# Kernel tuning notes

Measured on AMD Instinct MI355X. Metric: run time of the kernel, lower is better.

## Reference

```python
import jax, jax.numpy as jnp
import numpy as np

B, N, M, K = 8, 8192, 512, 32
C_IN, EMB = 3, 256
RADIUS2 = 0.1 * 0.1
EPS = 1e-5


def setup_inputs() -> dict:
    key = jax.random.key(0)
    ks = jax.random.split(key, 8)
    p = jax.random.uniform(ks[0], (B, N, 3), dtype=jnp.float32)           # coords in [0,1]^3
    x = jax.random.normal(ks[1], (B, C_IN, N), dtype=jnp.float32)          # features [B,C,N]
    def w(k, co, ci):
        return jax.random.normal(k, (co, ci), dtype=jnp.float32) / np.float32(np.sqrt(ci))
    return {
        "p": p, "x": x,
        # conv1: (6->256, BN+ReLU), (256->256, plain+bias)
        "W0": w(ks[2], EMB, 6), "g0": jnp.ones((EMB,), jnp.float32), "be0": jnp.zeros((EMB,), jnp.float32),
        "W1": w(ks[3], EMB, EMB), "b1": jnp.zeros((EMB,), jnp.float32),
        # conv2 (input doubled to 512): (512->512, BN+ReLU), (512->256, plain+bias)
        "W2": w(ks[4], 2 * EMB, 2 * EMB), "g2": jnp.ones((2 * EMB,), jnp.float32), "be2": jnp.zeros((2 * EMB,), jnp.float32),
        "W3": w(ks[5], EMB, 2 * EMB), "b3": jnp.zeros((EMB,), jnp.float32),
    }


def furthest_point_sample(p, m):
    # p: [B,N,3] -> idx [B,m] int32; starts at index 0 (matches CUDA FPS)
    b, n, _ = p.shape
    def step(carry, _):
        min_d, last = carry
        last_pt = jnp.take_along_axis(p, last[:, None, None], axis=1)     # [B,1,3]
        d = jnp.sum((p - last_pt) ** 2, axis=-1)                           # [B,N]
        min_d = jnp.minimum(min_d, d)
        nxt = jnp.argmax(min_d, axis=-1).astype(jnp.int32)
        return (min_d, nxt), last
    init = (jnp.full((b, n), 1e10, p.dtype), jnp.zeros((b,), jnp.int32))
    _, idx = jax.lax.scan(step, init, None, length=m)
    return idx.T                                                           # [B,m]


def ball_query(center_p, p, k, r2):
    # first-k-in-order points within radius; pad with first valid (center is always valid)
    d2 = jnp.sum((center_p[:, :, None, :] - p[:, None, :, :]) ** 2, axis=-1)  # [B,M,N]
    n = p.shape[1]
    keyv = jnp.where(d2 < r2, jnp.arange(n, dtype=jnp.int32), jnp.int32(n))   # [B,M,N]
    keys = jnp.sort(keyv, axis=-1)[..., :k]                                    # [B,M,K]
    valid = keys < n
    idx = jnp.where(valid, keys, keys[..., 0:1])
    return idx.astype(jnp.int32)


def bn_relu(f, g, b):
    # training-mode BatchNorm2d over (B, M, K) per channel, then ReLU
    mu = jnp.mean(f, axis=(0, 2, 3), keepdims=True)
    var = jnp.var(f, axis=(0, 2, 3), keepdims=True)
    fh = (f - mu) * jax.lax.rsqrt(var + EPS)
    return jax.nn.relu(fh * g[None, :, None, None] + b[None, :, None, None])


def reference(p, x, W0, g0, be0, W1, b1, W2, g2, be2, W3, b3):
    idx = furthest_point_sample(p, M)                                       # [B,M]
    center_p = jnp.take_along_axis(p, idx[:, :, None], axis=1)              # [B,M,3]
    gidx = ball_query(center_p, p, K, RADIUS2)                              # [B,M,K]
    grouped_xyz = jax.vmap(lambda pts, ix: pts[ix])(p, gidx)                # [B,M,K,3]
    dp = jnp.transpose(grouped_xyz - center_p[:, :, None, :], (0, 3, 1, 2))  # [B,3,M,K]
    fj = jax.vmap(lambda ft, ix: ft[:, ix])(x, gidx)                        # [B,C,M,K]
    center_x = jnp.take_along_axis(x, idx[:, None, :], axis=2)              # [B,C,M]
    f = jnp.concatenate([dp, fj - center_x[..., None]], axis=1)             # [B,6,M,K]  (dp_df)
    # conv1
    f = bn_relu(jnp.einsum('oc,bcmk->bomk', W0, f), g0, be0)
    f = jnp.einsum('oc,bcmk->bomk', W1, f) + b1[None, :, None, None]
    # mid max-pool concat
    fmax = jnp.max(f, axis=-1, keepdims=True)
    f = jnp.concatenate([jnp.broadcast_to(fmax, f.shape), f], axis=1)       # [B,512,M,K]
    # conv2
    f = bn_relu(jnp.einsum('oc,bcmk->bomk', W2, f), g2, be2)
    f = jnp.einsum('oc,bcmk->bomk', W3, f) + b3[None, :, None, None]
    out_f = jnp.max(f, axis=-1)                                             # [B,256,M]
    return (p, center_p, x, out_f)
```

## Files before the change

### kernel.cpp

```cpp
#include <hip/hip_runtime.h>

typedef unsigned short u16;
typedef unsigned int u32;
typedef unsigned long long u64;
typedef __bf16 bf16x8 __attribute__((ext_vector_type(8)));
typedef float v4f32 __attribute__((ext_vector_type(4)));

#define NP 8192
#define NM 512
#define LTOT 131072
#define NBM 4096
#define R2F 0.009999999776482582f

__device__ __forceinline__ float bf2f(u16 u) { return __uint_as_float(((u32)u) << 16); }
__device__ __forceinline__ u16 f2bf(float f) {
  u32 u = __float_as_uint(f);
  return (u16)((u + 0x7fffu + ((u >> 16) & 1u)) >> 16);
}
__device__ __forceinline__ void gl16(const void* g, void* l) {
  __builtin_amdgcn_global_load_lds((const __attribute__((address_space(1))) u32*)g,
                                   (__attribute__((address_space(3))) u32*)l, 16, 0, 0);
}

__device__ __forceinline__ u64 wave_max64_dpp(u64 k) {
#define DPP_STEP(CTRL) { \
    u32 lo_ = (u32)__builtin_amdgcn_update_dpp(0, (int)(u32)k, CTRL, 0xF, 0xF, true); \
    u32 hi_ = (u32)__builtin_amdgcn_update_dpp(0, (int)(u32)(k >> 32), CTRL, 0xF, 0xF, true); \
    u64 o_ = ((u64)hi_ << 32) | lo_; \
    if (o_ > k) k = o_; }
  DPP_STEP(0x111)
  DPP_STEP(0x112)
  DPP_STEP(0x114)
  DPP_STEP(0x118)
  DPP_STEP(0x142)
  DPP_STEP(0x143)
#undef DPP_STEP
  return k;
}

#define MFMA_COMPUTE_P(ASP, BSP) do { \
  bf16x8 a_[4], b_[4]; \
  _Pragma("unroll") \
  for (int mi_ = 0; mi_ < 4; ++mi_) a_[mi_] = *(const bf16x8*)&(ASP)[(wrow + mi_*16 + l15)*32 + l4*8]; \
  _Pragma("unroll") \
  for (int ni_ = 0; ni_ < 4; ++ni_) b_[ni_] = *(const bf16x8*)&(BSP)[(wcol + ni_*16 + l15)*32 + l4*8]; \
  _Pragma("unroll") \
  for (int mi_ = 0; mi_ < 4; ++mi_) { \
    _Pragma("unroll") \
    for (int ni_ = 0; ni_ < 4; ++ni_) \
      acc[mi_][ni_] = __builtin_amdgcn_mfma_f32_16x16x32_bf16(a_[mi_], b_[ni_], acc[mi_][ni_], 0, 0, 0); \
  } \
} while (0)
#define MFMA_COMPUTE() MFMA_COMPUTE_P(As, Bs)

__global__ __launch_bounds__(1024) void k_fps_prep(
    const float* __restrict__ p, const float* __restrict__ x,
    const float* __restrict__ W1, const float* __restrict__ W2, const float* __restrict__ W3,
    float* __restrict__ outP, float* __restrict__ outC, float* __restrict__ outX,
    u16* __restrict__ w1b, u16* __restrict__ w2b, u16* __restrict__ w3b,
    float* __restrict__ statz, int* __restrict__ idxb)
{
  const int tid = threadIdx.x;
  if (blockIdx.x >= 8) {
    for (size_t i = (size_t)(blockIdx.x - 8) * 1024 + tid; i < 855040; i += 104 * 1024) {
      if (i < 196608)      outP[i] = p[i];
      else if (i < 393216) outX[i - 196608] = x[i - 196608];
      else if (i < 458752) w1b[i - 393216] = f2bf(W1[i - 393216]);
      else if (i < 720896) w2b[i - 458752] = f2bf(W2[i - 458752]);
      else if (i < 851968) w3b[i - 720896] = f2bf(W3[i - 720896]);
      else                 statz[i - 851968] = 0.0f;
    }
    return;
  }
  const int b = blockIdx.x;
  const float* pb = p + (size_t)b * NP * 3;
  __shared__ float pl[NP * 3];
  __shared__ u64 slot[3];
  float px[8], py[8], pz[8], md[8];
  u32 nj[8];
  #pragma unroll
  for (int q = 0; q < 8; ++q) {
    int j = tid + (q << 10);
    float a0 = pb[j*3+0], a1 = pb[j*3+1], a2 = pb[j*3+2];
    px[q] = a0; py[q] = a1; pz[q] = a2; md[q] = 1e10f;
    nj[q] = ~(u32)j;
    pl[j*3+0] = a0; pl[j*3+1] = a1; pl[j*3+2] = a2;
  }
  if (tid < 3) slot[tid] = 0ull;
  __syncthreads();
  int last = 0;
  float* ctr = outC + (size_t)b * NM * 3;
  int* ip = idxb + b * NM;
  for (int s = 0; s < NM; ++s) {
    const int sl = s % 3;
    float lx = pl[last*3], ly = pl[last*3+1], lz = pl[last*3+2];
    if (tid == 0) {
      ip[s] = last; ctr[s*3] = lx; ctr[s*3+1] = ly; ctr[s*3+2] = lz;
      slot[(s+1) % 3] = 0ull;
    }
    #pragma unroll
    for (int q = 0; q < 8; ++q) {
      float dx = __fsub_rn(px[q], lx), dy = __fsub_rn(py[q], ly), dz = __fsub_rn(pz[q], lz);
      float d = __fadd_rn(__fadd_rn(__fmul_rn(dx,dx), __fmul_rn(dy,dy)), __fmul_rn(dz,dz));
      md[q] = fminf(md[q], d);
    }
    float t01 = fmaxf(md[0], md[1]), t23 = fmaxf(md[2], md[3]);
    float t45 = fmaxf(md[4], md[5]), t67 = fmaxf(md[6], md[7]);
    float tmax = fmaxf(fmaxf(t01, t23), fmaxf(t45, t67));
    u32 tb = __float_as_uint(tmax);
    u32 cand = 0;
    #pragma unroll
    for (int q = 0; q < 8; ++q) {
      u32 c = (__float_as_uint(md[q]) == tb) ? nj[q] : 0u;
      cand = c > cand ? c : cand;
    }
    u64 key = wave_max64_dpp(((u64)tb << 32) | (u64)cand);
    u32 klo = (u32)__builtin_amdgcn_readlane((int)(u32)key, 63);
    u32 khi = (u32)__builtin_amdgcn_readlane((int)(u32)(key >> 32), 63);
    if ((tid & 63) == 0)
      __hip_atomic_fetch_max(&slot[sl], ((u64)khi << 32) | klo,
                             __ATOMIC_RELAXED, __HIP_MEMORY_SCOPE_WORKGROUP);
    __syncthreads();
    last = (int)(~(u32)(slot[sl] & 0xffffffffull));
  }
}

__global__ __launch_bounds__(256) void k_group(
    const float* __restrict__ p, const float* __restrict__ x,
    const float* __restrict__ ctr, const int* __restrict__ idxb,
    u16* __restrict__ f0)
{
  const int tid = threadIdx.x, wv = tid >> 6, lane = tid & 63;
  const int cm = blockIdx.x * 4 + wv;
  const int b = cm >> 9;
  __shared__ int selS[4][33];
  volatile int* sel = selS[wv];
  const float cx0 = ctr[cm*3+0], cy0 = ctr[cm*3+1], cz0 = ctr[cm*3+2];
  const float* pb = p + (size_t)b * NP * 3;
  int cnt = 0;
  for (int ch = 0; ch < NP/64; ++ch) {
    if (cnt >= 32) break;
    int j = (ch << 6) + lane;
    float qx = pb[j*3], qy = pb[j*3+1], qz = pb[j*3+2];
    float dx = __fsub_rn(cx0,qx), dy = __fsub_rn(cy0,qy), dz = __fsub_rn(cz0,qz);
    float d2 = __fadd_rn(__fadd_rn(__fmul_rn(dx,dx),__fmul_rn(dy,dy)),__fmul_rn(dz,dz));
    bool pr = d2 < R2F;
    u64 msk = __ballot(pr);
    int pos = cnt + (int)__popcll(msk & ((1ull << lane) - 1ull));
    if (pr && pos < 32) sel[pos] = j;
    cnt += (int)__popcll(msk);
  }
  if (lane < 32) {
    int jj = (lane < cnt) ? sel[lane] : sel[0];
    const float* xb = x + (size_t)b * 3 * NP;
    int ic = idxb[cm];
    float gx = pb[jj*3], gy = pb[jj*3+1], gz = pb[jj*3+2];
    size_t col = (size_t)cm * 32 + lane;
    f0[0*(size_t)LTOT + col] = f2bf(gx - cx0);
    f0[1*(size_t)LTOT + col] = f2bf(gy - cy0);
    f0[2*(size_t)LTOT + col] = f2bf(gz - cz0);
    f0[3*(size_t)LTOT + col] = f2bf(xb[jj]      - xb[ic]);
    f0[4*(size_t)LTOT + col] = f2bf(xb[NP+jj]   - xb[NP+ic]);
    f0[5*(size_t)LTOT + col] = f2bf(xb[2*NP+jj] - xb[2*NP+ic]);
  }
}

__global__ __launch_bounds__(256) void k_cov(const u16* __restrict__ f0, float* __restrict__ cov)
{
  const int tid = threadIdx.x;
  const size_t col = (size_t)blockIdx.x * 256 + tid;
  float f[6];
  #pragma unroll
  for (int c = 0; c < 6; ++c) f[c] = bf2f(f0[(size_t)c * LTOT + col]);
  float v[27];
  int n = 0;
  #pragma unroll
  for (int c = 0; c < 6; ++c) v[n++] = f[c];
  #pragma unroll
  for (int i = 0; i < 6; ++i)
    #pragma unroll
    for (int j = i; j < 6; ++j) v[n++] = f[i] * f[j];
  #pragma unroll
  for (int k = 0; k < 27; ++k) {
    float s = v[k];
    #pragma unroll
    for (int off = 1; off < 64; off <<= 1) s += __shfl_xor(s, off);
    v[k] = s;
  }
  __shared__ float ls[27];
  if (tid < 27) ls[tid] = 0.f;
  __syncthreads();
  if ((tid & 63) == 0) {
    #pragma unroll
    for (int k = 0; k < 27; ++k) atomicAdd(&ls[k], v[k]);
  }
  __syncthreads();
  if (tid < 27) atomicAdd(&cov[tid], ls[tid]);
}

__global__ void k_fin1(const float* __restrict__ cov, const float* __restrict__ W0,
                       const float* __restrict__ g, const float* __restrict__ be,
                       float* __restrict__ S, float* __restrict__ T)
{
  int c = threadIdx.x;
  const float inv = 1.0f / 131072.0f;
  float w[6];
  #pragma unroll
  for (int k = 0; k < 6; ++k) w[k] = W0[c*6 + k];
  float mu = 0.f;
  #pragma unroll
  for (int k = 0; k < 6; ++k) mu = fmaf(w[k], cov[k], mu);
  mu *= inv;
  float e2 = 0.f;
  int n = 6;
  #pragma unroll
  for (int i = 0; i < 6; ++i)
    #pragma unroll
    for (int j = i; j < 6; ++j) {
      float coeff = (i == j) ? w[i]*w[j] : 2.f*w[i]*w[j];
      e2 = fmaf(coeff, cov[n++] * inv, e2);
    }
  float var = e2 - mu * mu;
  float s = g[c] / sqrtf(var + 1e-5f);
  S[c] = s; T[c] = be[c] - mu * s;
}

__global__ __launch_bounds__(256) void k_red(
    const float* __restrict__ pS, const float* __restrict__ pQ,
    const float* __restrict__ g, const float* __restrict__ be,
    float* __restrict__ S, float* __restrict__ T)
{
  const int c = blockIdx.x;
  const int tid = threadIdx.x;
  const int oTc = c >> 7, lc = c & 127;
  float s = 0.f, q = 0.f;
  for (int j = tid; j < 1024; j += 256) {
    size_t idx = (size_t)(j * 4 + oTc) * 128 + lc;
    s += pS[idx]; q += pQ[idx];
  }
  #pragma unroll
  for (int off = 1; off < 64; off <<= 1) { s += __shfl_xor(s, off); q += __shfl_xor(q, off); }
  __shared__ float ls[4], lq[4];
  if ((tid & 63) == 0) { ls[tid >> 6] = s; lq[tid >> 6] = q; }
  __syncthreads();
  if (tid == 0) {
    float ss = ls[0] + ls[1] + ls[2] + ls[3];
    float qq = lq[0] + lq[1] + lq[2] + lq[3];
    const float inv = 1.0f / 131072.0f;
    float mu = ss * inv;
    float var = qq * inv - mu * mu;
    float sc = g[c] / sqrtf(var + 1e-5f);
    S[c] = sc; T[c] = be[c] - mu * sc;
  }
}

__global__ __launch_bounds__(256) void k_g1(
    const u16* __restrict__ f0, const float* __restrict__ W0, u16* __restrict__ h1)
{
  __shared__ float w0l[1536];
  const int tid = threadIdx.x;
  for (int i = tid; i < 1536; i += 256) w0l[i] = W0[i];
  __syncthreads();
  const size_t col = (size_t)blockIdx.x * 256 + tid;
  float fin[6];
  #pragma unroll
  for (int c = 0; c < 6; ++c) fin[c] = bf2f(f0[(size_t)c * LTOT + col]);
  #pragma unroll
  for (int ob = 0; ob < 8; ++ob) {
    u32 w[16];
    #pragma unroll
    for (int pr2 = 0; pr2 < 16; ++pr2) {
      float v0 = 0.f, v1 = 0.f;
      int o0 = ob*32 + pr2*2;
      #pragma unroll
      for (int c = 0; c < 6; ++c) {
        v0 = fmaf(w0l[o0*6 + c], fin[c], v0);
        v1 = fmaf(w0l[(o0+1)*6 + c], fin[c], v1);
      }
      w[pr2] = (u32)f2bf(v0) | ((u32)f2bf(v1) << 16);
    }
    uint4* dst = (uint4*)(h1 + ((size_t)ob * LTOT + col) * 32);
    #pragma unroll
    for (int t4 = 0; t4 < 4; ++t4)
      dst[t4] = make_uint4(w[t4*4], w[t4*4+1], w[t4*4+2], w[t4*4+3]);
  }
}

__device__ __forceinline__ void xf_store(u16* Bs, int idx, uint4 q, int cb,
                                         const float* sS, const float* sT)
{
  u32 w[4]; u32 qa[4] = {q.x, q.y, q.z, q.w};
  #pragma unroll
  for (int t2 = 0; t2 < 4; ++t2) {
    float a  = fmaxf(fmaf(sS[cb + 2*t2],     bf2f((u16)(qa[t2] & 0xffffu)), sT[cb + 2*t2]), 0.f);
    float bv = fmaxf(fmaf(sS[cb + 2*t2 + 1], bf2f((u16)(qa[t2] >> 16)),     sT[cb + 2*t2 + 1]), 0.f);
    w[t2] = (u32)f2bf(a) | ((u32)f2bf(bv) << 16);
  }
  *(uint4*)&Bs[idx * 8] = make_uint4(w[0], w[1], w[2], w[3]);
}

__global__ __launch_bounds__(256) void k_gemm2(
    const u16* __restrict__ wA, const u16* __restrict__ hin,
    const float* __restrict__ Sc, const float* __restrict__ Tc,
    const float* __restrict__ bias,
    u16* __restrict__ h2, u16* __restrict__ fmaxb)
{
  __shared__ alignas(16) u16 As[4096];
  __shared__ alignas(16) u16 Bs[4096];
  __shared__ float sS[256], sT[256];
  const int tid = threadIdx.x;
  sS[tid] = Sc[tid]; sT[tid] = Tc[tid];
  const int oT = blockIdx.x & 1, cT = blockIdx.x >> 1;
  const int lane = tid & 63, wv = tid >> 6;
  const int wrow = (wv >> 1) * 64, wcol = (wv & 1) * 64;
  const int l15 = lane & 15, l4 = lane >> 4;
  v4f32 acc[4][4];
  #pragma unroll
  for (int mi = 0; mi < 4; ++mi)
    #pragma unroll
    for (int ni = 0; ni < 4; ++ni) acc[mi][ni] = (v4f32){0.f,0.f,0.f,0.f};
  const int idx0 = tid, idx1 = 256 + tid;
  const int r0 = idx0 >> 2, sg0 = idx0 & 3, r1 = idx1 >> 2, sg1 = idx1 & 3;
  __syncthreads();
  for (int kt = 0; kt < 8; ++kt) {
    const size_t bb = (size_t)kt * LTOT + (size_t)cT * 128;
    uint4 q0 = *(const uint4*)(hin + (bb + r0) * 32 + sg0 * 8);
    uint4 q1 = *(const uint4*)(hin + (bb + r1) * 32 + sg1 * 8);
    if (kt) __syncthreads();
    gl16(wA + (size_t)(oT*128 + r0) * 256 + kt*32 + sg0*8, &As[idx0 * 8]);
    gl16(wA + (size_t)(oT*128 + r1) * 256 + kt*32 + sg1*8, &As[idx1 * 8]);
    xf_store(Bs, idx0, q0, kt*32 + sg0*8, sS, sT);
    xf_store(Bs, idx1, q1, kt*32 + sg1*8, sS, sT);
    asm volatile("s_waitcnt vmcnt(0)" ::: "memory");
    __syncthreads();
    MFMA_COMPUTE();
  }
  const int oB = oT*128 + wrow + l4*4;
  const int cB = cT*128 + wcol + l15;
  #pragma unroll
  for (int mi = 0; mi < 4; ++mi) {
    const float4 bv = *(const float4*)&bias[oB + mi*16];
    #pragma unroll
    for (int ni = 0; ni < 4; ++ni) {
      acc[mi][ni][0] += bv.x; acc[mi][ni][1] += bv.y;
      acc[mi][ni][2] += bv.z; acc[mi][ni][3] += bv.w;
    }
  }
  #pragma unroll
  for (int mi = 0; mi < 4; ++mi) {
    const int o = oB + mi*16;
    const size_t rb = (size_t)(o >> 5) * LTOT * 32 + (o & 31);
    #pragma unroll
    for (int ni = 0; ni < 4; ++ni) {
      ushort4 u; u.x = f2bf(acc[mi][ni][0]); u.y = f2bf(acc[mi][ni][1]);
      u.z = f2bf(acc[mi][ni][2]); u.w = f2bf(acc[mi][ni][3]);
      *(ushort4*)&h2[rb + (size_t)(cB + ni*16) * 32] = u;
    }
  }
  #pragma unroll
  for (int g = 0; g < 2; ++g) {
    const int bm = (cT*128 + wcol + g*32) >> 5;
    #pragma unroll
    for (int mi = 0; mi < 4; ++mi) {
      float a0 = fmaxf(acc[mi][2*g][0], acc[mi][2*g+1][0]);
      float a1 = fmaxf(acc[mi][2*g][1], acc[mi][2*g+1][1]);
      float a2 = fmaxf(acc[mi][2*g][2], acc[mi][2*g+1][2]);
      float a3 = fmaxf(acc[mi][2*g][3], acc[mi][2*g+1][3]);
      #pragma unroll
      for (int off = 1; off < 16; off <<= 1) {
        a0 = fmaxf(a0, __shfl_xor(a0, off));
        a1 = fmaxf(a1, __shfl_xor(a1, off));
        a2 = fmaxf(a2, __shfl_xor(a2, off));
        a3 = fmaxf(a3, __shfl_xor(a3, off));
      }
      if (l15 == 0) {
        const int o = oB + mi*16;
        ushort4 u; u.x=f2bf(a0); u.y=f2bf(a1); u.z=f2bf(a2); u.w=f2bf(a3);
        *(ushort4*)&fmaxb[((size_t)(o >> 5) * NBM + bm) * 32 + (o & 31)] = u;
      }
    }
  }
}

__global__ __launch_bounds__(256) void k_fmb(
    const u16* __restrict__ wA, const u16* __restrict__ fmaxb, float* __restrict__ fmb)
{
  __shared__ alignas(16) u16 As[4096];
  __shared__ alignas(16) u16 Bs[4096];
  const int tid = threadIdx.x;
  const int oT = blockIdx.x & 3, cT = blockIdx.x >> 2;
  const int lane = tid & 63, wv = tid >> 6;
  const int wrow = (wv >> 1) * 64, wcol = (wv & 1) * 64;
  const int l15 = lane & 15, l4 = lane >> 4;
  v4f32 acc[4][4];
  #pragma unroll
  for (int mi = 0; mi < 4; ++mi)
    #pragma unroll
    for (int ni = 0; ni < 4; ++ni) acc[mi][ni] = (v4f32){0.f,0.f,0.f,0.f};
  const int idx0 = tid, idx1 = 256 + tid;
  const int r0 = idx0 >> 2, sg0 = idx0 & 3, r1 = idx1 >> 2, sg1 = idx1 & 3;
  for (int kt = 0; kt < 8; ++kt) {
    if (kt) __syncthreads();
    gl16(wA + (size_t)(oT*128 + r0) * 512 + kt*32 + sg0*8, &As[idx0 * 8]);
    gl16(wA + (size_t)(oT*128 + r1) * 512 + kt*32 + sg1*8, &As[idx1 * 8]);
    const size_t bb = (size_t)kt * NBM + (size_t)cT * 128;
    gl16(fmaxb + (bb + r0) * 32 + sg0 * 8, &Bs[idx0 * 8]);
    gl16(fmaxb + (bb + r1) * 32 + sg1 * 8, &Bs[idx1 * 8]);
    asm volatile("s_waitcnt vmcnt(0)" ::: "memory");
    __syncthreads();
    MFMA_COMPUTE();
  }
  const int oB = oT*128 + wrow + l4*4;
  const int cB = cT*128 + wcol + l15;
  #pragma unroll
  for (int mi = 0; mi < 4; ++mi) {
    const int o = oB + mi*16;
    #pragma unroll
    for (int ni = 0; ni < 4; ++ni) {
      const int colg = cB + ni*16;
      fmb[(size_t)(o+0)*NBM + colg] = acc[mi][ni][0];
      fmb[(size_t)(o+1)*NBM + colg] = acc[mi][ni][1];
      fmb[(size_t)(o+2)*NBM + colg] = acc[mi][ni][2];
      fmb[(size_t)(o+3)*NBM + colg] = acc[mi][ni][3];
    }
  }
}

__global__ __launch_bounds__(256) void k_gemm3(
    const u16* __restrict__ wA, const u16* __restrict__ hin,
    const float* __restrict__ fmb, u16* __restrict__ h3,
    float* __restrict__ pS, float* __restrict__ pQ)
{
  __shared__ alignas(16) u16 As[2][4096];
  __shared__ alignas(16) u16 Bs[2][4096];
  __shared__ float sAl[128], sQl[128];
  const int tid = threadIdx.x;
  const int oT = blockIdx.x & 3, cT = blockIdx.x >> 2;
  const int lane = tid & 63, wv = tid >> 6;
  const int wrow = (wv >> 1) * 64, wcol = (wv & 1) * 64;
  const int l15 = lane & 15, l4 = lane >> 4;
  if (tid < 128) { sAl[tid] = 0.f; sQl[tid] = 0.f; }
  v4f32 acc[4][4];
  #pragma unroll
  for (int mi = 0; mi < 4; ++mi)
    #pragma unroll
    for (int ni = 0; ni < 4; ++ni) acc[mi][ni] = (v4f32){0.f,0.f,0.f,0.f};
  const int idx0 = tid, idx1 = 256 + tid;
  const int r0 = idx0 >> 2, sg0 = idx0 & 3, r1 = idx1 >> 2, sg1 = idx1 & 3;
#define STAGE3(KT, BUF) do { \
    gl16(wA + (size_t)(oT*128 + r0) * 512 + 256 + (KT)*32 + sg0*8, &As[BUF][idx0 * 8]); \
    gl16(wA + (size_t)(oT*128 + r1) * 512 + 256 + (KT)*32 + sg1*8, &As[BUF][idx1 * 8]); \
    const size_t bb_ = (size_t)(KT) * LTOT + (size_t)cT * 128; \
    gl16(hin + (bb_ + r0) * 32 + sg0 * 8, &Bs[BUF][idx0 * 8]); \
    gl16(hin + (bb_ + r1) * 32 + sg1 * 8, &Bs[BUF][idx1 * 8]); \
  } while (0)
  STAGE3(0, 0);
  int cur = 0;
  for (int kt = 0; kt < 8; ++kt) {
    if (kt < 7) {
      STAGE3(kt + 1, cur ^ 1);
      asm volatile("s_waitcnt vmcnt(4)" ::: "memory");
    } else {
      asm volatile("s_waitcnt vmcnt(0)" ::: "memory");
    }
    asm volatile("s_barrier" ::: "memory");
    {
      const u16* Asp = As[cur];
      const u16* Bsp = Bs[cur];
      MFMA_COMPUTE_P(Asp, Bsp);
    }
    asm volatile("s_waitcnt lgkmcnt(0)" ::: "memory");
    asm volatile("s_barrier" ::: "memory");
    cur ^= 1;
  }
#undef STAGE3
  const int oB = oT*128 + wrow + l4*4;
  const int cB = cT*128 + wcol + l15;
  #pragma unroll
  for (int mi = 0; mi < 4; ++mi) {
    const int o = oB + mi*16;
    const size_t rb = (size_t)(o >> 5) * LTOT * 32 + (o & 31);
    float st[4] = {0.f,0.f,0.f,0.f}, sq[4] = {0.f,0.f,0.f,0.f};
    #pragma unroll
    for (int hf = 0; hf < 2; ++hf) {
      const int bm = (cT*128 + wcol + hf*32) >> 5;
      float e0 = fmb[(size_t)(o+0)*NBM + bm];
      float e1 = fmb[(size_t)(o+1)*NBM + bm];
      float e2 = fmb[(size_t)(o+2)*NBM + bm];
      float e3 = fmb[(size_t)(o+3)*NBM + bm];
      #pragma unroll
      for (int nn = 0; nn < 2; ++nn) {
        const int ni = hf*2 + nn;
        float v0 = acc[mi][ni][0] + e0;
        float v1 = acc[mi][ni][1] + e1;
        float v2 = acc[mi][ni][2] + e2;
        float v3 = acc[mi][ni][3] + e3;
        st[0] += v0; sq[0] = fmaf(v0, v0, sq[0]);
        st[1] += v1; sq[1] = fmaf(v1, v1, sq[1]);
        st[2] += v2; sq[2] = fmaf(v2, v2, sq[2]);
        st[3] += v3; sq[3] = fmaf(v3, v3, sq[3]);
        ushort4 u;
        u.x = f2bf(v0); u.y = f2bf(v1); u.z = f2bf(v2); u.w = f2bf(v3);
        *(ushort4*)&h3[rb + (size_t)(cB + ni*16) * 32] = u;
      }
    }
    #pragma unroll
    for (int e = 0; e < 4; ++e) {
      float s = st[e], q = sq[e];
      #pragma unroll
      for (int off = 1; off < 16; off <<= 1) {
        s += __shfl_xor(s, off);
        q += __shfl_xor(q, off);
      }
      if (l15 == 0) {
        const int lch = wrow + l4*4 + mi*16 + e;
        atomicAdd(&sAl[lch], s);
        atomicAdd(&sQl[lch], q);
      }
    }
  }
  __syncthreads();
  if (tid < 128) {
    pS[(size_t)blockIdx.x * 128 + tid] = sAl[tid];
    pQ[(size_t)blockIdx.x * 128 + tid] = sQl[tid];
  }
}

__global__ __launch_bounds__(256) void k_gemm4(
    const u16* __restrict__ wA, const u16* __restrict__ hin,
    const float* __restrict__ Sc, const float* __restrict__ Tc,
    const float* __restrict__ bias, float* __restrict__ outF)
{
  __shared__ alignas(16) u16 As[4096];
  __shared__ alignas(16) u16 Bs[4096];
  __shared__ float sS[512], sT[512];
  const int tid = threadIdx.x;
  sS[tid] = Sc[tid]; sT[tid] = Tc[tid];
  sS[tid+256] = Sc[tid+256]; sT[tid+256] = Tc[tid+256];
  const int oT = blockIdx.x & 1, cT = blockIdx.x >> 1;
  const int lane = tid & 63, wv = tid >> 6;
  const int wrow = (wv >> 1) * 64, wcol = (wv & 1) * 64;
  const int l15 = lane & 15, l4 = lane >> 4;
  v4f32 acc[4][4];
  #pragma unroll
  for (int mi = 0; mi < 4; ++mi)
    #pragma unroll
    for (int ni = 0; ni < 4; ++ni) acc[mi][ni] = (v4f32){0.f,0.f,0.f,0.f};
  const int idx0 = tid, idx1 = 256 + tid;
  const int r0 = idx0 >> 2, sg0 = idx0 & 3, r1 = idx1 >> 2, sg1 = idx1 & 3;
  __syncthreads();
  for (int kt = 0; kt < 16; ++kt) {
    const size_t bb = (size_t)kt * LTOT + (size_t)cT * 128;
    uint4 q0 = *(const uint4*)(hin + (bb + r0) * 32 + sg0 * 8);
    uint4 q1 = *(const uint4*)(hin + (bb + r1) * 32 + sg1 * 8);
    if (kt) __syncthreads();
    gl16(wA + (size_t)(oT*128 + r0) * 512 + kt*32 + sg0*8, &As[idx0 * 8]);
    gl16(wA + (size_t)(oT*128 + r1) * 512 + kt*32 + sg1*8, &As[idx1 * 8]);
    xf_store(Bs, idx0, q0, kt*32 + sg0*8, sS, sT);
    xf_store(Bs, idx1, q1, kt*32 + sg1*8, sS, sT);
    asm volatile("s_waitcnt vmcnt(0)" ::: "memory");
    __syncthreads();
    MFMA_COMPUTE();
  }
  const int oB = oT*128 + wrow + l4*4;
  #pragma unroll
  for (int mi = 0; mi < 4; ++mi) {
    const float4 bv = *(const float4*)&bias[oB + mi*16];
    #pragma unroll
    for (int ni = 0; ni < 4; ++ni) {
      acc[mi][ni][0] += bv.x; acc[mi][ni][1] += bv.y;
      acc[mi][ni][2] += bv.z; acc[mi][ni][3] += bv.w;
    }
  }
  #pragma unroll
  for (int g = 0; g < 2; ++g) {
    const int bm = (cT*128 + wcol + g*32) >> 5;
    const int bI = bm >> 9, mm = bm & 511;
    #pragma unroll
    for (int mi = 0; mi < 4; ++mi) {
      float a0 = fmaxf(acc[mi][2*g][0], acc[mi][2*g+1][0]);
      float a1 = fmaxf(acc[mi][2*g][1], acc[mi][2*g+1][1]);
      float a2 = fmaxf(acc[mi][2*g][2], acc[mi][2*g+1][2]);
      float a3 = fmaxf(acc[mi][2*g][3], acc[mi][2*g+1][3]);
      #pragma unroll
      for (int off = 1; off < 16; off <<= 1) {
        a0 = fmaxf(a0, __shfl_xor(a0, off));
        a1 = fmaxf(a1, __shfl_xor(a1, off));
        a2 = fmaxf(a2, __shfl_xor(a2, off));
        a3 = fmaxf(a3, __shfl_xor(a3, off));
      }
      if (l15 == 0) {
        const int o = oB + mi*16;
        outF[((size_t)bI*256 + o+0)*512 + mm] = a0;
        outF[((size_t)bI*256 + o+1)*512 + mm] = a1;
        outF[((size_t)bI*256 + o+2)*512 + mm] = a2;
        outF[((size_t)bI*256 + o+3)*512 + mm] = a3;
      }
    }
  }
}

extern "C" void kernel_launch(void* const* d_in, const int* in_sizes, int n_in,
                              void* d_out, int out_size, void* d_ws, size_t ws_size,
                              hipStream_t stream)
{
  (void)in_sizes; (void)n_in; (void)out_size; (void)ws_size;
  const float* p   = (const float*)d_in[0];
  const float* x   = (const float*)d_in[1];
  const float* W0  = (const float*)d_in[2];
  const float* g0  = (const float*)d_in[3];
  const float* be0 = (const float*)d_in[4];
  const float* W1  = (const float*)d_in[5];
  const float* b1  = (const float*)d_in[6];
  const float* W2  = (const float*)d_in[7];
  const float* g2  = (const float*)d_in[8];
  const float* be2 = (const float*)d_in[9];
  const float* W3  = (const float*)d_in[10];
  const float* b3  = (const float*)d_in[11];
  float* out  = (float*)d_out;
  float* outP = out;
  float* outC = out + 196608;
  float* outX = out + 208896;
  float* outF = out + 405504;
  char* ws = (char*)d_ws;
  u16* h2    = (u16*)(ws);
  u16* h3    = (u16*)(ws + 67108864);
  u16* h1    = h3;
  u16* f0    = (u16*)(ws + 201326592);
  u16* fmaxb = (u16*)(ws + 202899456);
  float* fmb = (float*)(ws + 204996608);
  u16* w1b   = (u16*)(ws + 213385216);
  u16* w2b   = (u16*)(ws + 213516288);
  u16* w3b   = (u16*)(ws + 214040576);
  int* idxb  = (int*)(ws + 214302720);
  float* statz = (float*)(ws + 214319104);
  float* cov  = statz;
  float* s0 = statz + 1536;   float* t0 = statz + 1792;
  float* s2 = statz + 2048;   float* t2 = statz + 2560;
  float* pS  = (float*)(ws + 214331392);
  float* pQ  = (float*)(ws + 216428544);

  k_fps_prep<<<112, 1024, 0, stream>>>(p, x, W1, W2, W3, outP, outC, outX,
                                       w1b, w2b, w3b, statz, idxb);
  k_group<<<1024, 256, 0, stream>>>(p, x, outC, idxb, f0);
  k_cov<<<512, 256, 0, stream>>>(f0, cov);
  k_fin1<<<1, 256, 0, stream>>>(cov, W0, g0, be0, s0, t0);
  k_g1<<<512, 256, 0, stream>>>(f0, W0, h1);
  k_gemm2<<<2048, 256, 0, stream>>>(w1b, h1, s0, t0, b1, h2, fmaxb);
  k_fmb<<<128, 256, 0, stream>>>(w2b, fmaxb, fmb);
  k_gemm3<<<4096, 256, 0, stream>>>(w2b, h2, fmb, h3, pS, pQ);
  k_red<<<512, 256, 0, stream>>>(pS, pQ, g2, be2, s2, t2);
  k_gemm4<<<2048, 256, 0, stream>>>(w3b, h3, s2, t2, b3, outF);
}
```

Measured before the change: 806.9 us.

## Fuse first conv into second GEMM, shrink FPS blocks, drop gemm3 double buffering

The 6->256 first conv (k_g1) is folded into the B-tile producer of the 256->256 GEMM, so each block recomputes its h1 tile from f0 and W0 in registers instead of writing and rereading a large bf16 intermediate. FPS now runs with 512 threads per block and 16 points per thread instead of 1024 threads and 8, which reduces waves taking part in the per-step barrier and atomic reduction. The gemm3 double-buffered LDS pipeline is replaced by a single-buffered load-wait-compute loop, trading copy/compute overlap for lower LDS use and possibly higher occupancy. The fused kernel recomputes conv1 once per output tile, because each column tile is processed by two oT blocks.

```diff
diff --git a/kernel.cpp b/kernel.cpp
--- a/kernel.cpp
+++ b/kernel.cpp
@@ -38,12 +38,12 @@
   return k;
 }
 
-#define MFMA_COMPUTE_P(ASP, BSP) do { \
+#define MFMA_COMPUTE() do { \
   bf16x8 a_[4], b_[4]; \
   _Pragma("unroll") \
-  for (int mi_ = 0; mi_ < 4; ++mi_) a_[mi_] = *(const bf16x8*)&(ASP)[(wrow + mi_*16 + l15)*32 + l4*8]; \
+  for (int mi_ = 0; mi_ < 4; ++mi_) a_[mi_] = *(const bf16x8*)&As[(wrow + mi_*16 + l15)*32 + l4*8]; \
   _Pragma("unroll") \
-  for (int ni_ = 0; ni_ < 4; ++ni_) b_[ni_] = *(const bf16x8*)&(BSP)[(wcol + ni_*16 + l15)*32 + l4*8]; \
+  for (int ni_ = 0; ni_ < 4; ++ni_) b_[ni_] = *(const bf16x8*)&Bs[(wcol + ni_*16 + l15)*32 + l4*8]; \
   _Pragma("unroll") \
   for (int mi_ = 0; mi_ < 4; ++mi_) { \
     _Pragma("unroll") \
@@ -51,9 +51,8 @@
       acc[mi_][ni_] = __builtin_amdgcn_mfma_f32_16x16x32_bf16(a_[mi_], b_[ni_], acc[mi_][ni_], 0, 0, 0); \
   } \
 } while (0)
-#define MFMA_COMPUTE() MFMA_COMPUTE_P(As, Bs)
-
-__global__ __launch_bounds__(1024) void k_fps_prep(
+
+__global__ __launch_bounds__(512) void k_fps_prep(
     const float* __restrict__ p, const float* __restrict__ x,
     const float* __restrict__ W1, const float* __restrict__ W2, const float* __restrict__ W3,
     float* __restrict__ outP, float* __restrict__ outC, float* __restrict__ outX,
@@ -62,7 +61,7 @@
 {
   const int tid = threadIdx.x;
   if (blockIdx.x >= 8) {
-    for (size_t i = (size_t)(blockIdx.x - 8) * 1024 + tid; i < 855040; i += 104 * 1024) {
+    for (size_t i = (size_t)(blockIdx.x - 8) * 512 + tid; i < 855040; i += 208 * 512) {
       if (i < 196608)      outP[i] = p[i];
       else if (i < 393216) outX[i - 196608] = x[i - 196608];
       else if (i < 458752) w1b[i - 393216] = f2bf(W1[i - 393216]);
@@ -76,11 +75,11 @@
   const float* pb = p + (size_t)b * NP * 3;
   __shared__ float pl[NP * 3];
   __shared__ u64 slot[3];
-  float px[8], py[8], pz[8], md[8];
-  u32 nj[8];
-  #pragma unroll
-  for (int q = 0; q < 8; ++q) {
-    int j = tid + (q << 10);
+  float px[16], py[16], pz[16], md[16];
+  u32 nj[16];
+  #pragma unroll
+  for (int q = 0; q < 16; ++q) {
+    int j = tid + (q << 9);
     float a0 = pb[j*3+0], a1 = pb[j*3+1], a2 = pb[j*3+2];
     px[q] = a0; py[q] = a1; pz[q] = a2; md[q] = 1e10f;
     nj[q] = ~(u32)j;
@@ -99,18 +98,20 @@
       slot[(s+1) % 3] = 0ull;
     }
     #pragma unroll
-    for (int q = 0; q < 8; ++q) {
+    for (int q = 0; q < 16; ++q) {
       float dx = __fsub_rn(px[q], lx), dy = __fsub_rn(py[q], ly), dz = __fsub_rn(pz[q], lz);
       float d = __fadd_rn(__fadd_rn(__fmul_rn(dx,dx), __fmul_rn(dy,dy)), __fmul_rn(dz,dz));
       md[q] = fminf(md[q], d);
     }
-    float t01 = fmaxf(md[0], md[1]), t23 = fmaxf(md[2], md[3]);
-    float t45 = fmaxf(md[4], md[5]), t67 = fmaxf(md[6], md[7]);
-    float tmax = fmaxf(fmaxf(t01, t23), fmaxf(t45, t67));
+    float t0 = fmaxf(fmaxf(md[0], md[1]),  fmaxf(md[2], md[3]));
+    float t1 = fmaxf(fmaxf(md[4], md[5]),  fmaxf(md[6], md[7]));
+    float t2 = fmaxf(fmaxf(md[8], md[9]),  fmaxf(md[10], md[11]));
+    float t3 = fmaxf(fmaxf(md[12], md[13]), fmaxf(md[14], md[15]));
+    float tmax = fmaxf(fmaxf(t0, t1), fmaxf(t2, t3));
     u32 tb = __float_as_uint(tmax);
     u32 cand = 0;
     #pragma unroll
-    for (int q = 0; q < 8; ++q) {
+    for (int q = 0; q < 16; ++q) {
       u32 c = (__float_as_uint(md[q]) == tb) ? nj[q] : 0u;
       cand = c > cand ? c : cand;
     }
@@ -254,38 +255,6 @@
   }
 }
 
-__global__ __launch_bounds__(256) void k_g1(
-    const u16* __restrict__ f0, const float* __restrict__ W0, u16* __restrict__ h1)
-{
-  __shared__ float w0l[1536];
-  const int tid = threadIdx.x;
-  for (int i = tid; i < 1536; i += 256) w0l[i] = W0[i];
-  __syncthreads();
-  const size_t col = (size_t)blockIdx.x * 256 + tid;
-  float fin[6];
-  #pragma unroll
-  for (int c = 0; c < 6; ++c) fin[c] = bf2f(f0[(size_t)c * LTOT + col]);
-  #pragma unroll
-  for (int ob = 0; ob < 8; ++ob) {
-    u32 w[16];
-    #pragma unroll
-    for (int pr2 = 0; pr2 < 16; ++pr2) {
-      float v0 = 0.f, v1 = 0.f;
-      int o0 = ob*32 + pr2*2;
-      #pragma unroll
-      for (int c = 0; c < 6; ++c) {
-        v0 = fmaf(w0l[o0*6 + c], fin[c], v0);
-        v1 = fmaf(w0l[(o0+1)*6 + c], fin[c], v1);
-      }
-      w[pr2] = (u32)f2bf(v0) | ((u32)f2bf(v1) << 16);
-    }
-    uint4* dst = (uint4*)(h1 + ((size_t)ob * LTOT + col) * 32);
-    #pragma unroll
-    for (int t4 = 0; t4 < 4; ++t4)
-      dst[t4] = make_uint4(w[t4*4], w[t4*4+1], w[t4*4+2], w[t4*4+3]);
-  }
-}
-
 __device__ __forceinline__ void xf_store(u16* Bs, int idx, uint4 q, int cb,
                                          const float* sS, const float* sT)
 {
@@ -299,21 +268,30 @@
   *(uint4*)&Bs[idx * 8] = make_uint4(w[0], w[1], w[2], w[3]);
 }
 
-__global__ __launch_bounds__(256) void k_gemm2(
-    const u16* __restrict__ wA, const u16* __restrict__ hin,
+__global__ __launch_bounds__(256) void k_gemm12(
+    const u16* __restrict__ wA, const u16* __restrict__ f0,
+    const float* __restrict__ W0,
     const float* __restrict__ Sc, const float* __restrict__ Tc,
     const float* __restrict__ bias,
     u16* __restrict__ h2, u16* __restrict__ fmaxb)
 {
   __shared__ alignas(16) u16 As[4096];
   __shared__ alignas(16) u16 Bs[4096];
+  __shared__ float w0l[1536];
   __shared__ float sS[256], sT[256];
   const int tid = threadIdx.x;
   sS[tid] = Sc[tid]; sT[tid] = Tc[tid];
+  for (int i = tid; i < 1536; i += 256) w0l[i] = W0[i];
   const int oT = blockIdx.x & 1, cT = blockIdx.x >> 1;
   const int lane = tid & 63, wv = tid >> 6;
   const int wrow = (wv >> 1) * 64, wcol = (wv & 1) * 64;
   const int l15 = lane & 15, l4 = lane >> 4;
+  const int myc = tid >> 1;
+  const int ch0 = (tid & 1) * 16;
+  const size_t gcol = (size_t)cT * 128 + myc;
+  float fin[6];
+  #pragma unroll
+  for (int c = 0; c < 6; ++c) fin[c] = bf2f(f0[(size_t)c * LTOT + gcol]);
   v4f32 acc[4][4];
   #pragma unroll
   for (int mi = 0; mi < 4; ++mi)
@@ -323,14 +301,26 @@
   const int r0 = idx0 >> 2, sg0 = idx0 & 3, r1 = idx1 >> 2, sg1 = idx1 & 3;
   __syncthreads();
   for (int kt = 0; kt < 8; ++kt) {
-    const size_t bb = (size_t)kt * LTOT + (size_t)cT * 128;
-    uint4 q0 = *(const uint4*)(hin + (bb + r0) * 32 + sg0 * 8);
-    uint4 q1 = *(const uint4*)(hin + (bb + r1) * 32 + sg1 * 8);
     if (kt) __syncthreads();
     gl16(wA + (size_t)(oT*128 + r0) * 256 + kt*32 + sg0*8, &As[idx0 * 8]);
     gl16(wA + (size_t)(oT*128 + r1) * 256 + kt*32 + sg1*8, &As[idx1 * 8]);
-    xf_store(Bs, idx0, q0, kt*32 + sg0*8, sS, sT);
-    xf_store(Bs, idx1, q1, kt*32 + sg1*8, sS, sT);
+    u32 wp[8];
+    #pragma unroll
+    for (int j = 0; j < 16; j += 2) {
+      const int o0 = kt*32 + ch0 + j;
+      float v0 = 0.f, v1 = 0.f;
+      #pragma unroll
+      for (int c = 0; c < 6; ++c) {
+        v0 = fmaf(w0l[o0*6 + c], fin[c], v0);
+        v1 = fmaf(w0l[(o0+1)*6 + c], fin[c], v1);
+      }
+      float h0 = bf2f(f2bf(v0)), h1v = bf2f(f2bf(v1));
+      float a0 = fmaxf(fmaf(sS[o0],     h0,  sT[o0]),     0.f);
+      float a1 = fmaxf(fmaf(sS[o0 + 1], h1v, sT[o0 + 1]), 0.f);
+      wp[j >> 1] = (u32)f2bf(a0) | ((u32)f2bf(a1) << 16);
+    }
+    *(uint4*)&Bs[myc*32 + ch0]     = make_uint4(wp[0], wp[1], wp[2], wp[3]);
+    *(uint4*)&Bs[myc*32 + ch0 + 8] = make_uint4(wp[4], wp[5], wp[6], wp[7]);
     asm volatile("s_waitcnt vmcnt(0)" ::: "memory");
     __syncthreads();
     MFMA_COMPUTE();
@@ -431,8 +421,8 @@
     const float* __restrict__ fmb, u16* __restrict__ h3,
     float* __restrict__ pS, float* __restrict__ pQ)
 {
-  __shared__ alignas(16) u16 As[2][4096];
-  __shared__ alignas(16) u16 Bs[2][4096];
+  __shared__ alignas(16) u16 As[4096];
+  __shared__ alignas(16) u16 Bs[4096];
   __shared__ float sAl[128], sQl[128];
   const int tid = threadIdx.x;
   const int oT = blockIdx.x & 3, cT = blockIdx.x >> 2;
@@ -447,33 +437,17 @@
     for (int ni = 0; ni < 4; ++ni) acc[mi][ni] = (v4f32){0.f,0.f,0.f,0.f};
   const int idx0 = tid, idx1 = 256 + tid;
   const int r0 = idx0 >> 2, sg0 = idx0 & 3, r1 = idx1 >> 2, sg1 = idx1 & 3;
-#define STAGE3(KT, BUF) do { \
-    gl16(wA + (size_t)(oT*128 + r0) * 512 + 256 + (KT)*32 + sg0*8, &As[BUF][idx0 * 8]); \
-    gl16(wA + (size_t)(oT*128 + r1) * 512 + 256 + (KT)*32 + sg1*8, &As[BUF][idx1 * 8]); \
-    const size_t bb_ = (size_t)(KT) * LTOT + (size_t)cT * 128; \
-    gl16(hin + (bb_ + r0) * 32 + sg0 * 8, &Bs[BUF][idx0 * 8]); \
-    gl16(hin + (bb_ + r1) * 32 + sg1 * 8, &Bs[BUF][idx1 * 8]); \
-  } while (0)
-  STAGE3(0, 0);
-  int cur = 0;
   for (int kt = 0; kt < 8; ++kt) {
-    if (kt < 7) {
-      STAGE3(kt + 1, cur ^ 1);
-      asm volatile("s_waitcnt vmcnt(4)" ::: "memory");
-    } else {
-      asm volatile("s_waitcnt vmcnt(0)" ::: "memory");
-    }
-    asm volatile("s_barrier" ::: "memory");
-    {
-      const u16* Asp = As[cur];
-      const u16* Bsp = Bs[cur];
-      MFMA_COMPUTE_P(Asp, Bsp);
-    }
-    asm volatile("s_waitcnt lgkmcnt(0)" ::: "memory");
-    asm volatile("s_barrier" ::: "memory");
-    cur ^= 1;
-  }
-#undef STAGE3
+    if (kt) __syncthreads();
+    gl16(wA + (size_t)(oT*128 + r0) * 512 + 256 + kt*32 + sg0*8, &As[idx0 * 8]);
+    gl16(wA + (size_t)(oT*128 + r1) * 512 + 256 + kt*32 + sg1*8, &As[idx1 * 8]);
+    const size_t bb = (size_t)kt * LTOT + (size_t)cT * 128;
+    gl16(hin + (bb + r0) * 32 + sg0 * 8, &Bs[idx0 * 8]);
+    gl16(hin + (bb + r1) * 32 + sg1 * 8, &Bs[idx1 * 8]);
+    asm volatile("s_waitcnt vmcnt(0)" ::: "memory");
+    __syncthreads();
+    MFMA_COMPUTE();
+  }
   const int oB = oT*128 + wrow + l4*4;
   const int cB = cT*128 + wcol + l15;
   #pragma unroll
@@ -625,7 +599,6 @@
   char* ws = (char*)d_ws;
   u16* h2    = (u16*)(ws);
   u16* h3    = (u16*)(ws + 67108864);
-  u16* h1    = h3;
   u16* f0    = (u16*)(ws + 201326592);
   u16* fmaxb = (u16*)(ws + 202899456);
   float* fmb = (float*)(ws + 204996608);
@@ -640,13 +613,12 @@
   float* pS  = (float*)(ws + 214331392);
   float* pQ  = (float*)(ws + 216428544);
 
-  k_fps_prep<<<112, 1024, 0, stream>>>(p, x, W1, W2, W3, outP, outC, outX,
-                                       w1b, w2b, w3b, statz, idxb);
+  k_fps_prep<<<216, 512, 0, stream>>>(p, x, W1, W2, W3, outP, outC, outX,
+                                      w1b, w2b, w3b, statz, idxb);
   k_group<<<1024, 256, 0, stream>>>(p, x, outC, idxb, f0);
   k_cov<<<512, 256, 0, stream>>>(f0, cov);
   k_fin1<<<1, 256, 0, stream>>>(cov, W0, g0, be0, s0, t0);
-  k_g1<<<512, 256, 0, stream>>>(f0, W0, h1);
-  k_gemm2<<<2048, 256, 0, stream>>>(w1b, h1, s0, t0, b1, h2, fmaxb);
+  k_gemm12<<<2048, 256, 0, stream>>>(w1b, f0, W0, s0, t0, b1, h2, fmaxb);
   k_fmb<<<128, 256, 0, stream>>>(w2b, fmaxb, fmb);
   k_gemm3<<<4096, 256, 0, stream>>>(w2b, h2, fmb, h3, pS, pQ);
   k_red<<<512, 256, 0, stream>>>(pS, pQ, g2, be2, s2, t2);
```

Result: faster. 775.5 us (-3.9%).
